# Kernel optimization log

Measured on AMD Instinct MI355X. Metric: run time of the kernel, lower is better.

Reference implementation:

```python
import jax, jax.numpy as jnp
import numpy as np

V, E, H, O = 32000, 512, 1024, 8   # vocab, embed_dim, hidden_dim, output_dim
B, T = 64, 512
PAD = 1  # padding_idx=1 in nn.Embedding


def setup_inputs() -> dict:
    key = jax.random.key(0)
    ks = jax.random.split(key, 8)
    s = 1.0 / np.sqrt(H)  # torch LSTM init scale
    x = jax.random.randint(ks[0], (B, T), 0, V)
    W_emb = jax.random.normal(ks[1], (V, E), dtype=jnp.float32)
    W_emb = W_emb.at[PAD].set(0.0)  # padding row is zero
    W_ih = jax.random.uniform(ks[2], (4 * H, E), jnp.float32, -s, s)
    W_hh = jax.random.uniform(ks[3], (4 * H, H), jnp.float32, -s, s)
    b_ih = jax.random.uniform(ks[4], (4 * H,), jnp.float32, -s, s)
    b_hh = jax.random.uniform(ks[5], (4 * H,), jnp.float32, -s, s)
    W_out = jax.random.uniform(ks[6], (O, H), jnp.float32, -s, s)
    b_out = jax.random.uniform(ks[7], (O,), jnp.float32, -s, s)
    return {"x": x, "W_emb": W_emb, "W_ih": W_ih, "W_hh": W_hh,
            "b_ih": b_ih, "b_hh": b_hh, "W_out": W_out, "b_out": b_out}


def _lstm_scan(emb_tbe, W_ih, W_hh, b_ih, b_hh):
    # emb_tbe: [T, B, E] -> hidden states [T, B, H]; torch gate order i,f,g,o
    Hh = W_hh.shape[1]
    b = b_ih + b_hh

    def step(carry, x_t):
        h, c = carry
        z = x_t @ W_ih.T + h @ W_hh.T + b  # [B, 4H]
        i, f, g, o = jnp.split(z, 4, axis=-1)
        c = jax.nn.sigmoid(f) * c + jax.nn.sigmoid(i) * jnp.tanh(g)
        h = jax.nn.sigmoid(o) * jnp.tanh(c)
        return (h, c), h

    h0 = jnp.zeros((emb_tbe.shape[1], Hh), emb_tbe.dtype)
    _, hs = jax.lax.scan(step, (h0, h0), emb_tbe)
    return hs


def reference(x, W_emb, W_ih, W_hh, b_ih, b_hh, W_out, b_out):
    Bsz = x.shape[0]
    emb = W_emb[x]                                   # [B, T, E]
    hs = _lstm_scan(emb.transpose(1, 0, 2), W_ih, W_hh, b_ih, b_hh)
    outputs = hs.transpose(1, 0, 2)                  # [B, T, H]
    pad = (x == PAD)
    outputs = jnp.where(pad[..., None], 0.0, outputs)  # masked_fill_
    lengths = jnp.sum(~pad, axis=1)                  # non-pad token counts
    final = outputs[jnp.arange(Bsz), lengths - 1]    # [B, H]
    # Dropout(p=0.5) is identity in eval mode
    logits = final @ W_out.T + b_out                 # [B, O]
    return logits
```

## Files before the change

### kernel.cpp

```cpp
#include <hip/hip_runtime.h>

typedef short bf16x8 __attribute__((ext_vector_type(8)));
typedef float f32x4  __attribute__((ext_vector_type(4)));
typedef unsigned long long u64;

#define MFMA16(a, b, c) __builtin_amdgcn_mfma_f32_16x16x32_bf16((a), (b), (c), 0, 0, 0)
#define AT_LD(p, o)    __hip_atomic_load((p), (o), __HIP_MEMORY_SCOPE_AGENT)
#define AT_ST(p, v, o) __hip_atomic_store((p), (v), (o), __HIP_MEMORY_SCOPE_AGENT)
#define AT_ADD(p, v, o) __hip_atomic_fetch_add((p), (v), (o), __HIP_MEMORY_SCOPE_AGENT)
#define WG_LD(p) __hip_atomic_load((p), __ATOMIC_ACQUIRE, __HIP_MEMORY_SCOPE_WORKGROUP)
#define WG_ST(p, v) __hip_atomic_store((p), (v), __ATOMIC_RELEASE, __HIP_MEMORY_SCOPE_WORKGROUP)

#define HSLOT 67584

__device__ __forceinline__ unsigned short f2bf(float f) {
  union { float f; unsigned u; } v; v.f = f;
  unsigned u = v.u;
  u += 0x7fffu + ((u >> 16) & 1u);
  return (unsigned short)(u >> 16);
}
__device__ __forceinline__ float bf2f(unsigned short h) {
  union { unsigned u; float f; } v; v.u = ((unsigned)h) << 16;
  return v.f;
}
__device__ __forceinline__ float sigf(float x) { return 1.f / (1.f + __expf(-x)); }
__device__ __forceinline__ float tanh_(float x) {
  x = fminf(15.f, fmaxf(-15.f, x));
  float e = __expf(2.f * x);
  return (e - 1.f) / (e + 1.f);
}

__device__ __forceinline__ void gbar_gemm(unsigned* bar, unsigned target) {
  __syncthreads();
  if (threadIdx.x == 0) {
    unsigned arr = AT_ADD(bar + 16512, 1u, __ATOMIC_RELEASE);
    if (arr == target * 128u - 1u) AT_ST(bar + 16576, target, __ATOMIC_RELEASE);
    while (AT_LD(bar + 16576, __ATOMIC_RELAXED) < target) __builtin_amdgcn_s_sleep(4);
    asm volatile("" ::: "memory");
  }
  __syncthreads();
}

__global__ void k_conv(const float* __restrict__ wih, const float* __restrict__ whh,
                       const float* __restrict__ wemb,
                       unsigned short* __restrict__ oih, unsigned short* __restrict__ ohh,
                       unsigned short* __restrict__ oemb) {
  const size_t NIH = (size_t)4096 * 512, NHH = (size_t)4096 * 1024;
  const size_t NE = (size_t)32000 * 512;
  size_t i0 = ((size_t)blockIdx.x * blockDim.x + threadIdx.x) * 4;
  size_t gs = (size_t)gridDim.x * blockDim.x * 4;
  for (size_t j = i0; j < NIH; j += gs) {
    float4 v = *(const float4*)(wih + j);
    uint2 pk;
    pk.x = (unsigned)f2bf(v.x) | ((unsigned)f2bf(v.y) << 16);
    pk.y = (unsigned)f2bf(v.z) | ((unsigned)f2bf(v.w) << 16);
    *(uint2*)(oih + j) = pk;
  }
  for (size_t j = i0; j < NHH; j += gs) {
    float4 v = *(const float4*)(whh + j);
    uint2 pk;
    pk.x = (unsigned)f2bf(v.x) | ((unsigned)f2bf(v.y) << 16);
    pk.y = (unsigned)f2bf(v.z) | ((unsigned)f2bf(v.w) << 16);
    *(uint2*)(ohh + j) = pk;
  }
  if (oemb)
    for (size_t j = i0; j < NE; j += gs) {
      float4 v = *(const float4*)(wemb + j);
      uint2 pk;
      pk.x = (unsigned)f2bf(v.x) | ((unsigned)f2bf(v.y) << 16);
      pk.y = (unsigned)f2bf(v.z) | ((unsigned)f2bf(v.w) << 16);
      *(uint2*)(oemb + j) = pk;
    }
}

__global__ void k_tsel(const int* __restrict__ x, int* __restrict__ tsel,
                       int* __restrict__ padsel) {
  int b = threadIdx.x >> 3, j = threadIdx.x & 7;
  int c = 0;
  for (int t = j * 64; t < j * 64 + 64; ++t) c += (x[b * 512 + t] != 1) ? 1 : 0;
  c += __shfl_xor(c, 1);
  c += __shfl_xor(c, 2);
  c += __shfl_xor(c, 4);
  if (j == 0) {
    int ts = (c - 1) & 511;
    tsel[b] = ts;
    padsel[b] = (x[b * 512 + ts] == 1) ? 1 : 0;
  }
}

__global__ void k_logits(const float* __restrict__ finalb, const float* __restrict__ Wout,
                         const float* __restrict__ bout, float* __restrict__ out) {
  int tid = threadIdx.x;
  for (int e = tid; e < 512; e += 256) {
    int b = e >> 3, o = e & 7;
    const float* f = finalb + (size_t)b * 1024;
    const float* w = Wout + (size_t)o * 1024;
    float s = 0.f;
    for (int k = 0; k < 1024; ++k) s += f[k] * w[k];
    out[e] = s + bout[o];
  }
}

struct SmemT {
  unsigned tok[2];
  unsigned cnt[2];
  union {
    struct { unsigned short sW[32][1032]; } rec;
    struct { unsigned short A[128][72]; unsigned short Bt[256][72]; } g;
    struct { unsigned short zs[128][136]; } zst;
  } u;
  unsigned short pad_force_one_wg_per_cu[8192];
};

__global__ __launch_bounds__(512, 1) void k_main(
    const int* __restrict__ x, const float* __restrict__ Wemb,
    const float* __restrict__ bih, const float* __restrict__ bhh,
    const unsigned short* __restrict__ Wihb, const unsigned short* __restrict__ Whhb,
    const unsigned short* __restrict__ wembb,
    unsigned short* __restrict__ hr, float* __restrict__ finalb,
    const int* __restrict__ tsel, const int* __restrict__ padsel,
    unsigned short* __restrict__ zxr, unsigned* __restrict__ bar, int chunkT,
    int nslot) {
  __shared__ SmemT smem;
  const int wg = blockIdx.x, tid = threadIdx.x;
  const int wave = tid >> 6, lane = tid & 63;
  const int l15 = lane & 15, lg = lane >> 4;
  unsigned* gemm_done = bar + 16640;
  const f32x4 fz = {0.f, 0.f, 0.f, 0.f};
  const int nChunks = 512 / chunkT;
  const size_t slotE = (size_t)chunkT * 64 * 4096;
  if (tid == 65535) smem.pad_force_one_wg_per_cu[0] = 0;

  if (wg < 128) {
    const int chain = wave >> 2;
    const int wv = wave & 3;
    const int btile = chain * 2 + (wv >> 1);
    const int mtile = wv & 1;
    const int my_b = btile * 16 + l15;
    const int col_local = 2 * lg + mtile;
    const int cg = wg * 8 + col_local;
    unsigned* myflags = bar + chain * 8192;
    unsigned* recdone = bar + 16704 + chain * 64;

    if (tid == 0) { smem.tok[0] = 0; smem.tok[1] = 0; smem.cnt[0] = 0; smem.cnt[1] = 0; }
    for (int e = tid; e < 32 * 64; e += 512) {
      int n = e >> 6, kq = (e & 63) << 4;
      int coll = (n < 16) ? 2 * (n >> 2) : 2 * ((n - 16) >> 2) + 1;
      int grow = (n & 3) * 1024 + wg * 8 + coll;
      *(uint4*)&smem.u.rec.sW[n][kq] = *(const uint4*)(Whhb + (size_t)grow * 1024 + kq);
      *(uint4*)&smem.u.rec.sW[n][kq + 8] =
          *(const uint4*)(Whhb + (size_t)grow * 1024 + kq + 8);
    }
    float biasv[4];
#pragma unroll
    for (int g = 0; g < 4; ++g) biasv[g] = bih[g * 1024 + cg] + bhh[g * 1024 + cg];
    const int my_tsel = tsel[my_b];
    const int my_pad = padsel[my_b];
    const size_t hwe = (size_t)btile * 16384 + (size_t)wg * 128 + (size_t)l15 * 8 + col_local;
    const size_t hre = (size_t)btile * 16384 + (size_t)lg * 128 + (size_t)l15 * 8;
    float cc = 0.f;

    {
      int e = wg * 512 + tid;
      if (e < 32768) AT_ST((unsigned*)hr + e, 0u, __ATOMIC_RELAXED);
    }
    __syncthreads();
    if (wv == 0 && lane == 0) AT_ST(myflags + wg * 64, 1u, __ATOMIC_RELAXED);

    for (int ch = 0; ch < nChunks; ++ch) {
      const int t0 = ch * chunkT;
      const unsigned short* zxbase = zxr + (size_t)(ch % nslot) * slotE;
      union { uint2 u2; unsigned short s[4]; } vv;
      bool vvload = true;

      for (int tl = 0; tl < chunkT; ++tl) {
        const int t = t0 + tl;
        const unsigned need = (unsigned)t + 1u;

        if (wv == 0) {
          if (tl == 0) {
            if (lane == 0) {
              while (AT_LD(gemm_done, __ATOMIC_RELAXED) < (unsigned)(ch + 1))
                __builtin_amdgcn_s_sleep(2);
              (void)AT_LD(gemm_done, __ATOMIC_ACQUIRE);
              asm volatile("" ::: "memory");
            }
          }
          const unsigned* f0 = myflags + (lane * 2) * 64;
          const unsigned* f1 = myflags + (lane * 2 + 1) * 64;
          for (;;) {
            int ok = (AT_LD(f0, __ATOMIC_RELAXED) >= need) &&
                     (AT_LD(f1, __ATOMIC_RELAXED) >= need);
            if (__all(ok)) break;
            __builtin_amdgcn_s_sleep(1);
          }
          if (lane == 0) WG_ST(&smem.tok[chain], need);
        } else {
          while (WG_LD(&smem.tok[chain]) < need) __builtin_amdgcn_s_sleep(1);
        }
        asm volatile("" ::: "memory");

        if (vvload) {
          vv.u2 = *(const uint2*)(zxbase + (size_t)(tl * 64 + my_b) * 4096 + cg * 4);
          vvload = false;
        }

        const unsigned short* hp = hr + (size_t)(t & 15) * HSLOT + hre;
        f32x4 r0 = fz;
        bf16x8 hf[32];
#pragma unroll
        for (int ks = 0; ks < 32; ++ks) hf[ks] = *(const bf16x8*)(hp + (size_t)ks * 512);
#pragma unroll
        for (int ks = 0; ks < 32; ++ks) {
          bf16x8 a0 = *(const bf16x8*)&smem.u.rec.sW[mtile * 16 + l15][ks * 32 + (lg << 3)];
          r0 = MFMA16(a0, hf[ks], r0);
        }

        float z0 = r0[0] + biasv[0] + bf2f(vv.s[0]);
        float z1 = r0[1] + biasv[1] + bf2f(vv.s[1]);
        float z2 = r0[2] + biasv[2] + bf2f(vv.s[2]);
        float z3 = r0[3] + biasv[3] + bf2f(vv.s[3]);
        cc = sigf(z1) * cc + sigf(z0) * tanh_(z2);
        float h = sigf(z3) * tanh_(cc);

        if (t == my_tsel) finalb[(size_t)my_b * 1024 + cg] = my_pad ? 0.f : h;
        __hip_atomic_store(hr + (size_t)((t + 1) & 15) * HSLOT + hwe, f2bf(h),
                           __ATOMIC_RELAXED, __HIP_MEMORY_SCOPE_AGENT);

        if (tl + 1 < chunkT) {
          vv.u2 = *(const uint2*)(zxbase + (size_t)((tl + 1) * 64 + my_b) * 4096 + cg * 4);
        }
        asm volatile("s_waitcnt vmcnt(0)" ::: "memory");
        if (lane == 0)
          __hip_atomic_fetch_add(&smem.cnt[chain], 1u, __ATOMIC_ACQ_REL,
                                 __HIP_MEMORY_SCOPE_WORKGROUP);
        if (wv == 0 && lane == 0) {
          while (__hip_atomic_load(&smem.cnt[chain], __ATOMIC_ACQUIRE,
                                   __HIP_MEMORY_SCOPE_WORKGROUP) < 4u * need)
            __builtin_amdgcn_s_sleep(1);
          AT_ST(myflags + wg * 64, need + 1u, __ATOMIC_RELAXED);
        }
      }
      if (wv == 0 && lane == 0) AT_ST(recdone, (unsigned)(ch + 1), __ATOMIC_RELAXED);
    }
  } else {
    const int gw = wg - 128;
    const int t2 = tid & 255;
    const int wv4 = (tid >> 6) & 3;
    unsigned* rdA = bar + 16704;
    unsigned* rdB = bar + 16768;
    unsigned gt = 0;
    for (int ch = 0; ch < nChunks; ++ch) {
      if (tid == 0 && ch >= nslot) {
        unsigned tgt = (unsigned)(ch - nslot + 1);
        for (;;) {
          unsigned a = AT_LD(rdA, __ATOMIC_RELAXED), b = AT_LD(rdB, __ATOMIC_RELAXED);
          if (a >= tgt && b >= tgt) break;
          __builtin_amdgcn_s_sleep(8);
        }
        asm volatile("" ::: "memory");
      }
      __syncthreads();
      const int t0 = ch * chunkT;
      unsigned short* zx = zxr + (size_t)(ch % nslot) * slotE;
      const int pmN = chunkT >> 1;
      const int npatch = pmN * 16;
      for (int p = gw; p < npatch; p += 128) {
        const int pm = p % pmN;
        const int n0 = (p / pmN) * 256;
        f32x4 acc[8][4];
#pragma unroll
        for (int mt = 0; mt < 8; ++mt)
#pragma unroll
          for (int nt = 0; nt < 4; ++nt) acc[mt][nt] = fz;
        for (int kc = 0; kc < 512; kc += 64) {
          __syncthreads();
          {
            int r = t2 >> 1, half = (t2 & 1) << 5;
            int tl = pm * 2 + (r >> 6), b = r & 63;
            int erow = x[b * 512 + t0 + tl];
            if (wembb) {
              const unsigned short* srcp = wembb + (size_t)erow * 512 + kc + half;
#pragma unroll
              for (int j = 0; j < 32; j += 8)
                *(uint4*)&smem.u.g.A[r][half + j] = *(const uint4*)(srcp + j);
            } else {
              const float* srcp = Wemb + (size_t)erow * 512 + kc + half;
#pragma unroll
              for (int j = 0; j < 32; j += 4) {
                float4 v = *(const float4*)(srcp + j);
                uint2 pk;
                pk.x = (unsigned)f2bf(v.x) | ((unsigned)f2bf(v.y) << 16);
                pk.y = (unsigned)f2bf(v.z) | ((unsigned)f2bf(v.w) << 16);
                *(uint2*)&smem.u.g.A[r][half + j] = pk;
              }
            }
          }
          {
            int zcx = n0 + t2;
            int wrow = (zcx & 3) * 1024 + (zcx >> 2);
            const unsigned short* srcp = Wihb + (size_t)wrow * 512 + kc;
#pragma unroll
            for (int j = 0; j < 64; j += 8)
              *(uint4*)&smem.u.g.Bt[t2][j] = *(const uint4*)(srcp + j);
          }
          __syncthreads();
#pragma unroll
          for (int ks = 0; ks < 64; ks += 32) {
            bf16x8 af[8];
#pragma unroll
            for (int mt = 0; mt < 8; ++mt)
              af[mt] = *(const bf16x8*)&smem.u.g.A[mt * 16 + l15][ks + (lg << 3)];
#pragma unroll
            for (int nt = 0; nt < 4; ++nt) {
              bf16x8 bfr =
                  *(const bf16x8*)&smem.u.g.Bt[(wv4 * 4 + nt) * 16 + l15][ks + (lg << 3)];
#pragma unroll
              for (int mt = 0; mt < 8; ++mt)
                acc[mt][nt] = MFMA16(af[mt], bfr, acc[mt][nt]);
            }
          }
        }
#pragma unroll
        for (int h = 0; h < 2; ++h) {
          __syncthreads();
          if ((wv4 >> 1) == h) {
#pragma unroll
            for (int mt = 0; mt < 8; ++mt)
#pragma unroll
              for (int nt = 0; nt < 4; ++nt)
#pragma unroll
                for (int r = 0; r < 4; ++r)
                  smem.u.zst.zs[mt * 16 + (lg << 2) + r][(wv4 & 1) * 64 + nt * 16 + l15] =
                      f2bf(acc[mt][nt][r]);
          }
          __syncthreads();
          int m = t2 >> 1, qq = (t2 & 1) << 6;
          int tl2 = pm * 2 + (m >> 6), bb = m & 63;
          unsigned short* dst = zx + ((size_t)(tl2 * 64 + bb)) * 4096 + n0 + h * 128 + qq;
#pragma unroll
          for (int j = 0; j < 64; j += 8)
            *(uint4*)(dst + j) = *(const uint4*)&smem.u.zst.zs[m][qq + j];
        }
      }
      gbar_gemm(bar, ++gt);
      if (wg == 128 && tid == 0) AT_ST(gemm_done, gt, __ATOMIC_RELAXED);
    }
  }
}

extern "C" void kernel_launch(void* const* d_in, const int* in_sizes, int n_in,
                              void* d_out, int out_size, void* d_ws, size_t ws_size,
                              hipStream_t stream) {
  (void)in_sizes; (void)n_in; (void)out_size;
  const int*   x    = (const int*)  d_in[0];
  const float* Wemb = (const float*)d_in[1];
  const float* Wih  = (const float*)d_in[2];
  const float* Whh  = (const float*)d_in[3];
  const float* bih  = (const float*)d_in[4];
  const float* bhh  = (const float*)d_in[5];
  const float* Wout = (const float*)d_in[6];
  const float* bout = (const float*)d_in[7];
  float* out = (float*)d_out;
  char* ws = (char*)d_ws;

  constexpr size_t OFF_WIH = 0;
  constexpr size_t OFF_WHH = OFF_WIH + (size_t)4096 * 512 * 2;
  constexpr size_t OFF_HR  = OFF_WHH + (size_t)4096 * 1024 * 2;
  constexpr size_t OFF_FIN = OFF_HR + (size_t)16 * HSLOT * 2;
  constexpr size_t OFF_TS  = OFF_FIN + (size_t)64 * 1024 * 4;
  constexpr size_t OFF_PS  = OFF_TS + 4096;
  constexpr size_t OFF_BAR = OFF_PS + 4096;
  constexpr size_t OFF_WEB = OFF_BAR + 73728;
  constexpr size_t WEB_SZ  = (size_t)32000 * 512 * 2;
  constexpr size_t SLOT_SZ = (size_t)16 * 64 * 4096 * 2;

  int chunkT = 16;
  bool wbf = true;
  int nslot = 2;
  if (OFF_WEB + WEB_SZ + 2 * SLOT_SZ <= ws_size) {
    nslot = (int)((ws_size - OFF_WEB - WEB_SZ) / SLOT_SZ);
    if (nslot > 32) nslot = 32;
  } else if (OFF_WEB + 2 * SLOT_SZ <= ws_size) {
    wbf = false;
    nslot = (int)((ws_size - OFF_WEB) / SLOT_SZ);
    if (nslot > 32) nslot = 32;
  } else {
    wbf = false;
    while (chunkT > 2 &&
           OFF_WEB + (size_t)2 * chunkT * 64 * 4096 * 2 > ws_size)
      chunkT >>= 1;
  }
  const size_t OFF_ZX = OFF_WEB + (wbf ? WEB_SZ : 0);

  unsigned short* wihb  = (unsigned short*)(ws + OFF_WIH);
  unsigned short* whhb  = (unsigned short*)(ws + OFF_WHH);
  unsigned short* hr    = (unsigned short*)(ws + OFF_HR);
  float* finalb         = (float*)(ws + OFF_FIN);
  int* tsel             = (int*)(ws + OFF_TS);
  int* padsel           = (int*)(ws + OFF_PS);
  unsigned* bar         = (unsigned*)(ws + OFF_BAR);
  unsigned short* wembb = wbf ? (unsigned short*)(ws + OFF_WEB) : (unsigned short*)nullptr;
  unsigned short* zxr   = (unsigned short*)(ws + OFF_ZX);

  hipMemsetAsync(ws + OFF_BAR, 0, 73728, stream);
  k_conv<<<2048, 256, 0, stream>>>(Wih, Whh, Wemb, wihb, whhb, wembb);
  k_tsel<<<1, 512, 0, stream>>>(x, tsel, padsel);
  k_main<<<256, 512, 0, stream>>>(x, Wemb, bih, bhh, wihb, whhb, wembb, hr, finalb,
                                  tsel, padsel, zxr, bar, chunkT, nslot);
  k_logits<<<1, 256, 0, stream>>>(finalb, Wout, bout, out);
}
```

Measured before the change: 2.911 ms.

## Replace per-workgroup token handoff with per-wave global flags across four independent chains

The recurrent workgroups previously used two chains of four waves, each coordinated by a shared-memory token and a counter, with one wave polling global flags and publishing for the whole workgroup. Now each pair of waves forms its own batch chain (four chains per workgroup). Every wave polls the peer flags directly and publishes its own per-wave flag as soon as its h store drains. The goal is to remove intra-workgroup serialization and handoff latency from the per-timestep critical path, at the cost of four times as many global flag polls per step and a larger barrier region.

```diff
diff --git a/kernel.cpp b/kernel.cpp
--- a/kernel.cpp
+++ b/kernel.cpp
@@ -8,8 +8,6 @@
 #define AT_LD(p, o)    __hip_atomic_load((p), (o), __HIP_MEMORY_SCOPE_AGENT)
 #define AT_ST(p, v, o) __hip_atomic_store((p), (v), (o), __HIP_MEMORY_SCOPE_AGENT)
 #define AT_ADD(p, v, o) __hip_atomic_fetch_add((p), (v), (o), __HIP_MEMORY_SCOPE_AGENT)
-#define WG_LD(p) __hip_atomic_load((p), __ATOMIC_ACQUIRE, __HIP_MEMORY_SCOPE_WORKGROUP)
-#define WG_ST(p, v) __hip_atomic_store((p), (v), __ATOMIC_RELEASE, __HIP_MEMORY_SCOPE_WORKGROUP)
 
 #define HSLOT 67584
 
@@ -33,9 +31,9 @@
 __device__ __forceinline__ void gbar_gemm(unsigned* bar, unsigned target) {
   __syncthreads();
   if (threadIdx.x == 0) {
-    unsigned arr = AT_ADD(bar + 16512, 1u, __ATOMIC_RELEASE);
-    if (arr == target * 128u - 1u) AT_ST(bar + 16576, target, __ATOMIC_RELEASE);
-    while (AT_LD(bar + 16576, __ATOMIC_RELAXED) < target) __builtin_amdgcn_s_sleep(4);
+    unsigned arr = AT_ADD(bar + 65536, 1u, __ATOMIC_RELEASE);
+    if (arr == target * 128u - 1u) AT_ST(bar + 65600, target, __ATOMIC_RELEASE);
+    while (AT_LD(bar + 65600, __ATOMIC_RELAXED) < target) __builtin_amdgcn_s_sleep(4);
     asm volatile("" ::: "memory");
   }
   __syncthreads();
@@ -102,8 +100,6 @@
 }
 
 struct SmemT {
-  unsigned tok[2];
-  unsigned cnt[2];
   union {
     struct { unsigned short sW[32][1032]; } rec;
     struct { unsigned short A[128][72]; unsigned short Bt[256][72]; } g;
@@ -125,24 +121,26 @@
   const int wg = blockIdx.x, tid = threadIdx.x;
   const int wave = tid >> 6, lane = tid & 63;
   const int l15 = lane & 15, lg = lane >> 4;
-  unsigned* gemm_done = bar + 16640;
+  unsigned* gemm_done = bar + 65664;
   const f32x4 fz = {0.f, 0.f, 0.f, 0.f};
   const int nChunks = 512 / chunkT;
   const size_t slotE = (size_t)chunkT * 64 * 4096;
   if (tid == 65535) smem.pad_force_one_wg_per_cu[0] = 0;
 
   if (wg < 128) {
-    const int chain = wave >> 2;
-    const int wv = wave & 3;
-    const int btile = chain * 2 + (wv >> 1);
-    const int mtile = wv & 1;
-    const int my_b = btile * 16 + l15;
+    const int chain = wave >> 1;
+    const int mtile = wave & 1;
+    const int my_b = chain * 16 + l15;
     const int col_local = 2 * lg + mtile;
     const int cg = wg * 8 + col_local;
-    unsigned* myflags = bar + chain * 8192;
-    unsigned* recdone = bar + 16704 + chain * 64;
-
-    if (tid == 0) { smem.tok[0] = 0; smem.tok[1] = 0; smem.cnt[0] = 0; smem.cnt[1] = 0; }
+    unsigned* chflags = bar + chain * 16384;
+    unsigned* myflag  = chflags + (wg * 2 + mtile) * 64;
+    unsigned* recdone = bar + 65728 + chain * 64;
+    const unsigned* pf0 = chflags + (lane * 4 + 0) * 64;
+    const unsigned* pf1 = chflags + (lane * 4 + 1) * 64;
+    const unsigned* pf2 = chflags + (lane * 4 + 2) * 64;
+    const unsigned* pf3 = chflags + (lane * 4 + 3) * 64;
+
     for (int e = tid; e < 32 * 64; e += 512) {
       int n = e >> 6, kq = (e & 63) << 4;
       int coll = (n < 16) ? 2 * (n >> 2) : 2 * ((n - 16) >> 2) + 1;
@@ -156,8 +154,8 @@
     for (int g = 0; g < 4; ++g) biasv[g] = bih[g * 1024 + cg] + bhh[g * 1024 + cg];
     const int my_tsel = tsel[my_b];
     const int my_pad = padsel[my_b];
-    const size_t hwe = (size_t)btile * 16384 + (size_t)wg * 128 + (size_t)l15 * 8 + col_local;
-    const size_t hre = (size_t)btile * 16384 + (size_t)lg * 128 + (size_t)l15 * 8;
+    const size_t hwe = (size_t)chain * 16384 + (size_t)wg * 128 + (size_t)l15 * 8 + col_local;
+    const size_t hre = (size_t)chain * 16384 + (size_t)lg * 128 + (size_t)l15 * 8;
     float cc = 0.f;
 
     {
@@ -165,45 +163,35 @@
       if (e < 32768) AT_ST((unsigned*)hr + e, 0u, __ATOMIC_RELAXED);
     }
     __syncthreads();
-    if (wv == 0 && lane == 0) AT_ST(myflags + wg * 64, 1u, __ATOMIC_RELAXED);
+    if (lane == 0) AT_ST(myflag, 1u, __ATOMIC_RELAXED);
 
     for (int ch = 0; ch < nChunks; ++ch) {
       const int t0 = ch * chunkT;
       const unsigned short* zxbase = zxr + (size_t)(ch % nslot) * slotE;
+
+      if (lane == 0) {
+        while (AT_LD(gemm_done, __ATOMIC_RELAXED) < (unsigned)(ch + 1))
+          __builtin_amdgcn_s_sleep(2);
+      }
+      (void)AT_LD(gemm_done, __ATOMIC_ACQUIRE);
+      asm volatile("" ::: "memory");
+
       union { uint2 u2; unsigned short s[4]; } vv;
-      bool vvload = true;
+      vv.u2 = *(const uint2*)(zxbase + (size_t)(0 * 64 + my_b) * 4096 + cg * 4);
 
       for (int tl = 0; tl < chunkT; ++tl) {
         const int t = t0 + tl;
         const unsigned need = (unsigned)t + 1u;
 
-        if (wv == 0) {
-          if (tl == 0) {
-            if (lane == 0) {
-              while (AT_LD(gemm_done, __ATOMIC_RELAXED) < (unsigned)(ch + 1))
-                __builtin_amdgcn_s_sleep(2);
-              (void)AT_LD(gemm_done, __ATOMIC_ACQUIRE);
-              asm volatile("" ::: "memory");
-            }
-          }
-          const unsigned* f0 = myflags + (lane * 2) * 64;
-          const unsigned* f1 = myflags + (lane * 2 + 1) * 64;
-          for (;;) {
-            int ok = (AT_LD(f0, __ATOMIC_RELAXED) >= need) &&
-                     (AT_LD(f1, __ATOMIC_RELAXED) >= need);
-            if (__all(ok)) break;
-            __builtin_amdgcn_s_sleep(1);
-          }
-          if (lane == 0) WG_ST(&smem.tok[chain], need);
-        } else {
-          while (WG_LD(&smem.tok[chain]) < need) __builtin_amdgcn_s_sleep(1);
+        for (;;) {
+          int ok = (AT_LD(pf0, __ATOMIC_RELAXED) >= need) &&
+                   (AT_LD(pf1, __ATOMIC_RELAXED) >= need) &&
+                   (AT_LD(pf2, __ATOMIC_RELAXED) >= need) &&
+                   (AT_LD(pf3, __ATOMIC_RELAXED) >= need);
+          if (__all(ok)) break;
+          __builtin_amdgcn_s_sleep(1);
         }
         asm volatile("" ::: "memory");
-
-        if (vvload) {
-          vv.u2 = *(const uint2*)(zxbase + (size_t)(tl * 64 + my_b) * 4096 + cg * 4);
-          vvload = false;
-        }
 
         const unsigned short* hp = hr + (size_t)(t & 15) * HSLOT + hre;
         f32x4 r0 = fz;
@@ -227,35 +215,29 @@
         __hip_atomic_store(hr + (size_t)((t + 1) & 15) * HSLOT + hwe, f2bf(h),
                            __ATOMIC_RELAXED, __HIP_MEMORY_SCOPE_AGENT);
 
+        asm volatile("s_waitcnt vmcnt(0)" ::: "memory");
+        if (lane == 0) AT_ST(myflag, need + 1u, __ATOMIC_RELAXED);
+
         if (tl + 1 < chunkT) {
           vv.u2 = *(const uint2*)(zxbase + (size_t)((tl + 1) * 64 + my_b) * 4096 + cg * 4);
         }
-        asm volatile("s_waitcnt vmcnt(0)" ::: "memory");
-        if (lane == 0)
-          __hip_atomic_fetch_add(&smem.cnt[chain], 1u, __ATOMIC_ACQ_REL,
-                                 __HIP_MEMORY_SCOPE_WORKGROUP);
-        if (wv == 0 && lane == 0) {
-          while (__hip_atomic_load(&smem.cnt[chain], __ATOMIC_ACQUIRE,
-                                   __HIP_MEMORY_SCOPE_WORKGROUP) < 4u * need)
-            __builtin_amdgcn_s_sleep(1);
-          AT_ST(myflags + wg * 64, need + 1u, __ATOMIC_RELAXED);
-        }
       }
-      if (wv == 0 && lane == 0) AT_ST(recdone, (unsigned)(ch + 1), __ATOMIC_RELAXED);
+      if (mtile == 0 && lane == 0) AT_ST(recdone, (unsigned)(ch + 1), __ATOMIC_RELAXED);
     }
   } else {
     const int gw = wg - 128;
     const int t2 = tid & 255;
     const int wv4 = (tid >> 6) & 3;
-    unsigned* rdA = bar + 16704;
-    unsigned* rdB = bar + 16768;
     unsigned gt = 0;
     for (int ch = 0; ch < nChunks; ++ch) {
       if (tid == 0 && ch >= nslot) {
         unsigned tgt = (unsigned)(ch - nslot + 1);
         for (;;) {
-          unsigned a = AT_LD(rdA, __ATOMIC_RELAXED), b = AT_LD(rdB, __ATOMIC_RELAXED);
-          if (a >= tgt && b >= tgt) break;
+          unsigned a = AT_LD(bar + 65728, __ATOMIC_RELAXED);
+          unsigned b = AT_LD(bar + 65792, __ATOMIC_RELAXED);
+          unsigned c = AT_LD(bar + 65856, __ATOMIC_RELAXED);
+          unsigned d = AT_LD(bar + 65920, __ATOMIC_RELAXED);
+          if (a >= tgt && b >= tgt && c >= tgt && d >= tgt) break;
           __builtin_amdgcn_s_sleep(8);
         }
         asm volatile("" ::: "memory");
@@ -371,7 +353,8 @@
   constexpr size_t OFF_TS  = OFF_FIN + (size_t)64 * 1024 * 4;
   constexpr size_t OFF_PS  = OFF_TS + 4096;
   constexpr size_t OFF_BAR = OFF_PS + 4096;
-  constexpr size_t OFF_WEB = OFF_BAR + 73728;
+  constexpr size_t BAR_SZ  = 266240;
+  constexpr size_t OFF_WEB = OFF_BAR + BAR_SZ;
   constexpr size_t WEB_SZ  = (size_t)32000 * 512 * 2;
   constexpr size_t SLOT_SZ = (size_t)16 * 64 * 4096 * 2;
 
@@ -403,7 +386,7 @@
   unsigned short* wembb = wbf ? (unsigned short*)(ws + OFF_WEB) : (unsigned short*)nullptr;
   unsigned short* zxr   = (unsigned short*)(ws + OFF_ZX);
 
-  hipMemsetAsync(ws + OFF_BAR, 0, 73728, stream);
+  hipMemsetAsync(ws + OFF_BAR, 0, BAR_SZ, stream);
   k_conv<<<2048, 256, 0, stream>>>(Wih, Whh, Wemb, wihb, whhb, wembb);
   k_tsel<<<1, 512, 0, stream>>>(x, tsel, padsel);
   k_main<<<256, 512, 0, stream>>>(x, Wemb, bih, bhh, wihb, whhb, wembb, hr, finalb,
```

Measured after the change: 5.136 ms. +76.4%, slower.
